# Performance work log

Hardware: AMD Instinct MI355X
Metric: run time of the kernel (lower is better)

The kernel has to match this reference:

```python
import jax, jax.numpy as jnp
import numpy as np

N = 100000   # nodes
E = 1250000  # edges per graph
D = 64       # in_feats
H = 64       # hidden_dim
C = 129      # num_classes
EPS = 1e-5


def setup_inputs() -> dict:
    key = jax.random.key(0)
    ks = jax.random.split(key, 32)
    nrm = lambda k, s: jax.random.normal(k, s, jnp.float32) * 0.05
    inp = {
        'node_features': jax.random.normal(ks[0], (N, D), jnp.float32),
        'm_src': jax.random.randint(ks[1], (E,), 0, N, jnp.int32),
        'm_dst': jax.random.randint(ks[2], (E,), 0, N, jnp.int32),
        'r_src': jax.random.randint(ks[3], (E,), 0, N, jnp.int32),
        'r_dst': jax.random.randint(ks[4], (E,), 0, N, jnp.int32),
    }
    i = 5
    for pre in ('soc', 'rt'):
        inp[pre + '_W1'] = nrm(ks[i], (D, H)); inp[pre + '_b1'] = jnp.zeros((H,), jnp.float32)
        inp[pre + '_g1'] = jnp.ones((H,), jnp.float32); inp[pre + '_bt1'] = jnp.zeros((H,), jnp.float32)
        inp[pre + '_W2'] = nrm(ks[i + 1], (H, H)); inp[pre + '_b2'] = jnp.zeros((H,), jnp.float32)
        inp[pre + '_g2'] = jnp.ones((H,), jnp.float32); inp[pre + '_bt2'] = jnp.zeros((H,), jnp.float32)
        i += 2
    inp['gW1'] = nrm(ks[i], (4 * H, H)); inp['gb1'] = jnp.zeros((H,), jnp.float32)
    inp['prelu_a'] = jnp.full((1,), 0.25, jnp.float32)
    inp['gW2'] = nrm(ks[i + 1], (H, H)); inp['gb2'] = jnp.zeros((H,), jnp.float32)
    inp['fcW'] = nrm(ks[i + 2], (H, C)); inp['fcb'] = jnp.zeros((C,), jnp.float32)
    return inp


def _gconv(h, src, dst, W, b):
    # DGL GraphConv, norm='both': D_out^{-1/2} (scatter-sum) D_in^{-1/2}, linear, ELU
    ones = jnp.ones(src.shape[0], jnp.float32)
    deg_o = jax.ops.segment_sum(ones, src, num_segments=N)
    deg_i = jax.ops.segment_sum(ones, dst, num_segments=N)
    ns = jax.lax.rsqrt(jnp.clip(deg_o, 1.0))
    nd = jax.lax.rsqrt(jnp.clip(deg_i, 1.0))
    agg = jax.ops.segment_sum((h * ns[:, None])[src], dst, num_segments=N)
    return jax.nn.elu((agg * nd[:, None]) @ W + b)


def _bn(x, g, b):
    mu = x.mean(0)
    v = x.var(0)
    return (x - mu) * jax.lax.rsqrt(v + EPS) * g + b


def _branch(x, src, dst, W1, b1, g1, bt1, W2, b2, g2, bt2):
    h = _bn(_gconv(x, src, dst, W1, b1), g1, bt1)
    return _bn(_gconv(h, src, dst, W2, b2), g2, bt2)


def reference(node_features, m_src, m_dst, r_src, r_dst,
              soc_W1, soc_b1, soc_g1, soc_bt1, soc_W2, soc_b2, soc_g2, soc_bt2,
              rt_W1, rt_b1, rt_g1, rt_bt1, rt_W2, rt_b2, rt_g2, rt_bt2,
              gW1, gb1, prelu_a, gW2, gb2, fcW, fcb):
    h1 = _branch(node_features, m_src, m_dst, soc_W1, soc_b1, soc_g1, soc_bt1, soc_W2, soc_b2, soc_g2, soc_bt2)
    h2 = _branch(node_features, r_src, r_dst, rt_W1, rt_b1, rt_g1, rt_bt1, rt_W2, rt_b2, rt_g2, rt_bt2)
    cat = jnp.concatenate([h1, h2, jnp.abs(h1 - h2), h1 * h2], axis=-1)
    z = cat @ gW1 + gb1
    z = jnp.where(z > 0, z, prelu_a * z)  # PReLU (single shared slope)
    gate = jax.nn.sigmoid(z @ gW2 + gb2)
    fused = gate * h1 + (1.0 - gate) * h2
    return fused @ fcW + fcb
```

## Files before the change

### kernel.cpp

```cpp
#include <hip/hip_runtime.h>
#include <math.h>

#define NN 100000
#define NE 1250000
#define HD 64
#define NCLS 129
#define NTILES 6250
#define GRID_T 782

#define NCHD 256
#define CHD ((NE + NCHD - 1) / NCHD)
#define NCHS 64
#define CHS ((NE + NCHS - 1) / NCHS)
#define SUBR 50000
#define NW2 12500
#define NHE2 ((NN + 1) * (size_t)HD)

typedef float f32x4 __attribute__((ext_vector_type(4)));
typedef short bf16x8 __attribute__((ext_vector_type(8)));

__device__ __forceinline__ short f2b(float f) {
    unsigned u = __builtin_bit_cast(unsigned, f);
    u += 0x7FFFu + ((u >> 16) & 1u);
    return (short)(u >> 16);
}
__device__ __forceinline__ float b2f(short s) {
    return __builtin_bit_cast(float, ((unsigned)(unsigned short)s) << 16);
}

__global__ __launch_bounds__(1024) void k_hist8(
    const int* __restrict__ idx0, const int* __restrict__ idx1,
    unsigned char* __restrict__ P8, int chunk, int nch) {
    __shared__ unsigned int hw[NW2];
    int b = blockIdx.x, s = blockIdx.y, g = blockIdx.z;
    const int* __restrict__ idx = g ? idx1 : idx0;
    for (int i = threadIdx.x; i < NW2; i += 1024) hw[i] = 0;
    __syncthreads();
    int lo = s * SUBR;
    int beg = b * chunk, end = beg + chunk;
    if (end > NE) end = NE;
    for (int i = beg + threadIdx.x; i < end; i += 1024) {
        int v = idx[i] - lo;
        if ((unsigned)v < (unsigned)SUBR)
            atomicAdd(&hw[v >> 2], 1u << ((v & 3) * 8));
    }
    __syncthreads();
    unsigned int* dst = (unsigned int*)(P8 + ((size_t)(g * nch + b)) * NN + lo);
    for (int i = threadIdx.x; i < NW2; i += 1024) dst[i] = hw[i];
}

__global__ void k_reduce8(unsigned int* __restrict__ Pd, const unsigned int* __restrict__ Ps,
                          float* __restrict__ ns, float* __restrict__ nd,
                          int* __restrict__ degi) {
    int w = blockIdx.x * 256 + threadIdx.x;
    if (w >= NN / 4) return;
    int g = blockIdx.y;
    Pd += (size_t)g * NCHD * (NN / 4);
    Ps += (size_t)g * NCHS * (NN / 4);
    ns += (size_t)g * NN; nd += (size_t)g * NN; degi += (size_t)g * NN;
    unsigned run = 0;
#pragma unroll 8
    for (int b = 0; b < NCHD; ++b) {
        size_t o = (size_t)b * (NN / 4) + w;
        unsigned v = Pd[o];
        Pd[o] = run;
        run += v;
    }
    unsigned so = 0;
#pragma unroll 8
    for (int b = 0; b < NCHS; ++b) so += Ps[(size_t)b * (NN / 4) + w];
#pragma unroll
    for (int j = 0; j < 4; ++j) {
        int din = (run >> (8 * j)) & 255;
        int dout = (so >> (8 * j)) & 255;
        int node = w * 4 + j;
        degi[node] = din;
        ns[node] = rsqrtf((float)(dout < 1 ? 1 : dout));
        nd[node] = rsqrtf((float)(din < 1 ? 1 : din));
    }
}

__global__ void k_scan_local(const int* __restrict__ deg, int* __restrict__ excl,
                             int* __restrict__ bsums) {
    __shared__ int sm[1024];
    int g = blockIdx.y;
    deg += (size_t)g * NN; excl += (size_t)g * (NN + 1); bsums += g * 1024;
    int t = threadIdx.x;
    int i = blockIdx.x * 1024 + t;
    int v = (i < NN) ? deg[i] : 0;
    sm[t] = v;
    __syncthreads();
    for (int ofs = 1; ofs < 1024; ofs <<= 1) {
        int x = (t >= ofs) ? sm[t - ofs] : 0;
        __syncthreads();
        sm[t] += x;
        __syncthreads();
    }
    if (i < NN) excl[i] = sm[t] - v;
    if (t == 1023) bsums[blockIdx.x] = sm[1023];
}

__global__ void k_scan_tops(int* __restrict__ bsums, int nb) {
    __shared__ int sm[1024];
    bsums += blockIdx.y * 1024;
    int t = threadIdx.x;
    int v = (t < nb) ? bsums[t] : 0;
    sm[t] = v;
    __syncthreads();
    for (int ofs = 1; ofs < 1024; ofs <<= 1) {
        int x = (t >= ofs) ? sm[t - ofs] : 0;
        __syncthreads();
        sm[t] += x;
        __syncthreads();
    }
    if (t < nb) bsums[t] = sm[t] - v;
}

__global__ void k_scan_add(int* __restrict__ excl, const int* __restrict__ bsums) {
    int g = blockIdx.y;
    excl += (size_t)g * (NN + 1); bsums += g * 1024;
    int i = blockIdx.x * blockDim.x + threadIdx.x;
    if (i < NN) excl[i] += bsums[i >> 10];
    if (i == 0) excl[NN] = NE;
}

__global__ __launch_bounds__(1024) void k_fill8(
    const int* __restrict__ d0, const int* __restrict__ d1,
    const int* __restrict__ s0, const int* __restrict__ s1,
    const int* __restrict__ rowptr, const unsigned char* __restrict__ Pofs,
    int* __restrict__ col) {
    __shared__ unsigned int cur[NW2];
    int b = blockIdx.x, s = blockIdx.y, g = blockIdx.z;
    const int* __restrict__ dst = g ? d1 : d0;
    const int* __restrict__ src = g ? s1 : s0;
    rowptr += (size_t)g * (NN + 1);
    col += (size_t)g * NE;
    const unsigned char* __restrict__ ofs = Pofs + ((size_t)(g * NCHD + b)) * NN;
    for (int i = threadIdx.x; i < NW2; i += 1024) cur[i] = 0;
    __syncthreads();
    int lo = s * SUBR;
    int beg = b * CHD, end = beg + CHD;
    if (end > NE) end = NE;
    for (int i = beg + threadIdx.x; i < end; i += 1024) {
        int d = dst[i] - lo;
        if ((unsigned)d < (unsigned)SUBR) {
            unsigned old = atomicAdd(&cur[d >> 2], 1u << ((d & 3) * 8));
            int r = (old >> ((d & 3) * 8)) & 255;
            int node = d + lo;
            col[rowptr[node] + (int)ofs[node] + r] = src[i];
        }
    }
}

__global__ void k_scale_nf(const float* __restrict__ nf, const float* __restrict__ ns,
                           short* __restrict__ T) {
    int i = blockIdx.x * blockDim.x + threadIdx.x;
    if (i >= (NN + 1) * 8) return;
    int g = blockIdx.y;
    ns += (size_t)g * NN; T += (size_t)g * NHE2;
    int node = i >> 3;
    short r[8];
    if (node == NN) {
#pragma unroll
        for (int j = 0; j < 8; ++j) r[j] = 0;
    } else {
        float s = ns[node];
        const float4* p = (const float4*)(nf + (size_t)i * 8);
        float4 a = p[0], b = p[1];
        r[0] = f2b(a.x * s); r[1] = f2b(a.y * s); r[2] = f2b(a.z * s); r[3] = f2b(a.w * s);
        r[4] = f2b(b.x * s); r[5] = f2b(b.y * s); r[6] = f2b(b.z * s); r[7] = f2b(b.w * s);
    }
    *(bf16x8*)(T + (size_t)i * 8) = *(bf16x8*)r;
}

__global__ __launch_bounds__(256) void k_gather(
    const short* __restrict__ tab, const float* __restrict__ nd,
    const int* __restrict__ rowptr, const int* __restrict__ col,
    short* __restrict__ out) {
    int w = (blockIdx.x * 256 + threadIdx.x) >> 6;
    int lane = threadIdx.x & 63;
    if (w >= NN) return;
    int g = blockIdx.y;
    tab += (size_t)g * NHE2; nd += (size_t)g * NN;
    rowptr += (size_t)g * (NN + 1); col += (size_t)g * NE; out += (size_t)g * NHE2;
    int grp = lane >> 4;
    int sub = lane & 15;
    int beg = rowptr[w], end = rowptr[w + 1];
    float a0 = 0.f, a1 = 0.f, a2 = 0.f, a3 = 0.f;
    for (int e0 = beg; e0 < end; e0 += 64) {
        int cnt = end - e0; if (cnt > 64) cnt = 64;
        int myc = (lane < cnt) ? col[e0 + lane] : NN;
        for (int j = 0; j < cnt; j += 16) {
#pragma unroll
            for (int u = 0; u < 4; ++u) {
                int c = __shfl(myc, j + u * 4 + grp, 64);
                uint2 v = *(const uint2*)(tab + (size_t)c * HD + sub * 4);
                a0 += __builtin_bit_cast(float, v.x << 16);
                a1 += __builtin_bit_cast(float, v.x & 0xffff0000u);
                a2 += __builtin_bit_cast(float, v.y << 16);
                a3 += __builtin_bit_cast(float, v.y & 0xffff0000u);
            }
        }
    }
    a0 += __shfl_xor(a0, 16, 64); a1 += __shfl_xor(a1, 16, 64);
    a2 += __shfl_xor(a2, 16, 64); a3 += __shfl_xor(a3, 16, 64);
    a0 += __shfl_xor(a0, 32, 64); a1 += __shfl_xor(a1, 32, 64);
    a2 += __shfl_xor(a2, 32, 64); a3 += __shfl_xor(a3, 32, 64);
    if (grp == 0) {
        float s = nd[w];
        unsigned r0 = ((unsigned)(unsigned short)f2b(a0 * s)) |
                      (((unsigned)(unsigned short)f2b(a1 * s)) << 16);
        unsigned r1 = ((unsigned)(unsigned short)f2b(a2 * s)) |
                      (((unsigned)(unsigned short)f2b(a3 * s)) << 16);
        uint2 r; r.x = r0; r.y = r1;
        *(uint2*)(out + (size_t)w * HD + sub * 4) = r;
    }
}

__global__ __launch_bounds__(256) void k_lin(
    const short* __restrict__ X, const float* __restrict__ Wa, const float* __restrict__ Wb,
    const float* __restrict__ ba, const float* __restrict__ bb,
    short* __restrict__ Y, float* __restrict__ stats) {
    __shared__ short sW[4096];
    __shared__ float sm2[128];
    int g = blockIdx.y;
    const float* W = g ? Wb : Wa;
    const float* bias = g ? bb : ba;
    X += (size_t)g * NHE2; Y += (size_t)g * NHE2; stats += (size_t)g * 128;
    int t = threadIdx.x;
    for (int i = t; i < 4096; i += 256) {
        int j = i & 7, l16i = (i >> 3) & 15, kgi = (i >> 7) & 3, kbi = (i >> 9) & 1, oti = (i >> 10) & 3;
        sW[i] = f2b(W[(kbi * 32 + kgi * 8 + j) * HD + oti * 16 + l16i]);
    }
    if (t < 128) sm2[t] = 0.f;
    __syncthreads();
    int lane = t & 63, wv = t >> 6, l16 = lane & 15, kg = lane >> 4;
    bf16x8 bfrag[2][4];
#pragma unroll
    for (int kb = 0; kb < 2; ++kb)
#pragma unroll
        for (int ot = 0; ot < 4; ++ot)
            bfrag[kb][ot] = *(const bf16x8*)&sW[((ot * 2 + kb) * 4 + kg) * 128 + l16 * 8];
    float bo[4];
#pragma unroll
    for (int ot = 0; ot < 4; ++ot) bo[ot] = bias[ot * 16 + l16];
    float ps[4] = {0.f, 0.f, 0.f, 0.f}, pq[4] = {0.f, 0.f, 0.f, 0.f};
    for (int tile = blockIdx.x * 4 + wv; tile < NTILES; tile += GRID_T * 4) {
        const short* xp = X + ((size_t)tile * 16 + l16) * HD + kg * 8;
        bf16x8 a0 = *(const bf16x8*)xp;
        bf16x8 a1 = *(const bf16x8*)(xp + 32);
        f32x4 acc[4];
#pragma unroll
        for (int ot = 0; ot < 4; ++ot) {
            acc[ot] = (f32x4){0.f, 0.f, 0.f, 0.f};
            acc[ot] = __builtin_amdgcn_mfma_f32_16x16x32_bf16(a0, bfrag[0][ot], acc[ot], 0, 0, 0);
            acc[ot] = __builtin_amdgcn_mfma_f32_16x16x32_bf16(a1, bfrag[1][ot], acc[ot], 0, 0, 0);
        }
#pragma unroll
        for (int ot = 0; ot < 4; ++ot) {
#pragma unroll
            for (int r = 0; r < 4; ++r) {
                float y = acc[ot][r] + bo[ot];
                y = y > 0.f ? y : expm1f(y);
                ps[ot] += y; pq[ot] += y * y;
                Y[((size_t)tile * 16 + kg * 4 + r) * HD + ot * 16 + l16] = f2b(y);
            }
        }
    }
#pragma unroll
    for (int ot = 0; ot < 4; ++ot) {
        atomicAdd(&sm2[ot * 16 + l16], ps[ot]);
        atomicAdd(&sm2[64 + ot * 16 + l16], pq[ot]);
    }
    __syncthreads();
    if (t < 128) atomicAdd(&stats[t], sm2[t]);
}

__global__ void k_bnb(const short* __restrict__ Y, short* __restrict__ O,
                      const float* __restrict__ stats,
                      const float* __restrict__ ga, const float* __restrict__ gb,
                      const float* __restrict__ bta, const float* __restrict__ btb,
                      const float* __restrict__ ns) {
    int i = blockIdx.x * blockDim.x + threadIdx.x;
    if (i >= (NN + 1) * 8) return;
    int gI = blockIdx.y;
    Y += (size_t)gI * NHE2; O += (size_t)gI * NHE2; stats += (size_t)gI * 128;
    const float* g = gI ? gb : ga;
    const float* bt = gI ? btb : bta;
    if (ns) ns += (size_t)gI * NN;
    int node = i >> 3;
    short r[8];
    if (node == NN) {
#pragma unroll
        for (int j = 0; j < 8; ++j) r[j] = 0;
    } else {
        int o0 = (i & 7) * 8;
        float extra = ns ? ns[node] : 1.f;
        bf16x8 v = *(const bf16x8*)(Y + (size_t)i * 8);
        const float invN = 1.f / (float)NN;
#pragma unroll
        for (int j = 0; j < 8; ++j) {
            int o = o0 + j;
            float mu = stats[o] * invN;
            float var = fmaxf(stats[64 + o] * invN - mu * mu, 0.f);
            float isd = rsqrtf(var + 1e-5f);
            float sc = g[o] * isd * extra;
            float sh = (bt[o] - mu * g[o] * isd) * extra;
            r[j] = f2b(b2f(v[j]) * sc + sh);
        }
    }
    *(bf16x8*)(O + (size_t)i * 8) = *(bf16x8*)r;
}

__global__ __launch_bounds__(256) void k_comb1(
    const short* __restrict__ H1, const short* __restrict__ H2,
    const float* __restrict__ W, const float* __restrict__ bias,
    const float* __restrict__ pa, short* __restrict__ Z) {
    __shared__ short sW[16384];
    int t = threadIdx.x;
    for (int i = t; i < 16384; i += 256) {
        int j = i & 7, l16i = (i >> 3) & 15, kgi = (i >> 7) & 3, kbi = (i >> 9) & 7, oti = (i >> 12) & 3;
        sW[i] = f2b(W[(kbi * 32 + kgi * 8 + j) * HD + oti * 16 + l16i]);
    }
    __syncthreads();
    int lane = t & 63, wv = t >> 6, l16 = lane & 15, kg = lane >> 4;
    float slope = pa[0];
    float bo[4];
#pragma unroll
    for (int ot = 0; ot < 4; ++ot) bo[ot] = bias[ot * 16 + l16];
    for (int tile = blockIdx.x * 4 + wv; tile < NTILES; tile += GRID_T * 4) {
        size_t rb = ((size_t)tile * 16 + l16) * HD + kg * 8;
        bf16x8 h1e = *(const bf16x8*)(H1 + rb);
        bf16x8 h1o = *(const bf16x8*)(H1 + rb + 32);
        bf16x8 h2e = *(const bf16x8*)(H2 + rb);
        bf16x8 h2o = *(const bf16x8*)(H2 + rb + 32);
        bf16x8 fe[8];
        fe[0] = h1e; fe[1] = h1o; fe[2] = h2e; fe[3] = h2o;
        short tabs[8], tprd[8];
#pragma unroll
        for (int j = 0; j < 8; ++j) {
            float a = b2f(h1e[j]), b = b2f(h2e[j]);
            tabs[j] = f2b(fabsf(a - b)); tprd[j] = f2b(a * b);
        }
        fe[4] = *(bf16x8*)tabs; fe[6] = *(bf16x8*)tprd;
#pragma unroll
        for (int j = 0; j < 8; ++j) {
            float a = b2f(h1o[j]), b = b2f(h2o[j]);
            tabs[j] = f2b(fabsf(a - b)); tprd[j] = f2b(a * b);
        }
        fe[5] = *(bf16x8*)tabs; fe[7] = *(bf16x8*)tprd;
        f32x4 acc[4];
#pragma unroll
        for (int ot = 0; ot < 4; ++ot) acc[ot] = (f32x4){0.f, 0.f, 0.f, 0.f};
#pragma unroll
        for (int kb = 0; kb < 8; ++kb)
#pragma unroll
            for (int ot = 0; ot < 4; ++ot) {
                bf16x8 bf = *(const bf16x8*)&sW[((ot * 8 + kb) * 4 + kg) * 128 + l16 * 8];
                acc[ot] = __builtin_amdgcn_mfma_f32_16x16x32_bf16(fe[kb], bf, acc[ot], 0, 0, 0);
            }
#pragma unroll
        for (int ot = 0; ot < 4; ++ot)
#pragma unroll
            for (int r = 0; r < 4; ++r) {
                float z = acc[ot][r] + bo[ot];
                z = z > 0.f ? z : slope * z;
                Z[((size_t)tile * 16 + kg * 4 + r) * HD + ot * 16 + l16] = f2b(z);
            }
    }
}

__global__ __launch_bounds__(256) void k_comb2(
    const short* __restrict__ Z, const float* __restrict__ W,
    const float* __restrict__ bias, short* __restrict__ G) {
    __shared__ short sW[4096];
    int t = threadIdx.x;
    for (int i = t; i < 4096; i += 256) {
        int j = i & 7, l16i = (i >> 3) & 15, kgi = (i >> 7) & 3, kbi = (i >> 9) & 1, oti = (i >> 10) & 3;
        sW[i] = f2b(W[(kbi * 32 + kgi * 8 + j) * HD + oti * 16 + l16i]);
    }
    __syncthreads();
    int lane = t & 63, wv = t >> 6, l16 = lane & 15, kg = lane >> 4;
    bf16x8 bfrag[2][4];
#pragma unroll
    for (int kb = 0; kb < 2; ++kb)
#pragma unroll
        for (int ot = 0; ot < 4; ++ot)
            bfrag[kb][ot] = *(const bf16x8*)&sW[((ot * 2 + kb) * 4 + kg) * 128 + l16 * 8];
    float bo[4];
#pragma unroll
    for (int ot = 0; ot < 4; ++ot) bo[ot] = bias[ot * 16 + l16];
    for (int tile = blockIdx.x * 4 + wv; tile < NTILES; tile += GRID_T * 4) {
        const short* xp = Z + ((size_t)tile * 16 + l16) * HD + kg * 8;
        bf16x8 a0 = *(const bf16x8*)xp;
        bf16x8 a1 = *(const bf16x8*)(xp + 32);
        f32x4 acc[4];
#pragma unroll
        for (int ot = 0; ot < 4; ++ot) {
            acc[ot] = (f32x4){0.f, 0.f, 0.f, 0.f};
            acc[ot] = __builtin_amdgcn_mfma_f32_16x16x32_bf16(a0, bfrag[0][ot], acc[ot], 0, 0, 0);
            acc[ot] = __builtin_amdgcn_mfma_f32_16x16x32_bf16(a1, bfrag[1][ot], acc[ot], 0, 0, 0);
        }
#pragma unroll
        for (int ot = 0; ot < 4; ++ot)
#pragma unroll
            for (int r = 0; r < 4; ++r) {
                float y = acc[ot][r] + bo[ot];
                float gate = 1.f / (1.f + expf(-y));
                G[((size_t)tile * 16 + kg * 4 + r) * HD + ot * 16 + l16] = f2b(gate);
            }
    }
}

__global__ __launch_bounds__(256) void k_fc(
    const short* __restrict__ G, const short* __restrict__ H1, const short* __restrict__ H2,
    const float* __restrict__ W, const float* __restrict__ bias,
    float* __restrict__ out) {
    __shared__ short sW[9216];
    int t = threadIdx.x;
    for (int i = t; i < 9216; i += 256) {
        int j = i & 7, l16i = (i >> 3) & 15, kgi = (i >> 7) & 3, kbi = (i >> 9) & 1, oti = i >> 10;
        int k = kbi * 32 + kgi * 8 + j, o = oti * 16 + l16i;
        sW[i] = (o < NCLS) ? f2b(W[k * NCLS + o]) : (short)0;
    }
    __syncthreads();
    int lane = t & 63, wv = t >> 6, l16 = lane & 15, kg = lane >> 4;
    float bo[9];
#pragma unroll
    for (int ot = 0; ot < 9; ++ot) {
        int o = ot * 16 + l16;
        bo[ot] = (o < NCLS) ? bias[o] : 0.f;
    }
    for (int tile = blockIdx.x * 4 + wv; tile < NTILES; tile += GRID_T * 4) {
        size_t rb = ((size_t)tile * 16 + l16) * HD;
        f32x4 acc[9];
#pragma unroll
        for (int ot = 0; ot < 9; ++ot) acc[ot] = (f32x4){0.f, 0.f, 0.f, 0.f};
#pragma unroll
        for (int kb = 0; kb < 2; ++kb) {
            int koff = kb * 32 + kg * 8;
            bf16x8 gv  = *(const bf16x8*)(G + rb + koff);
            bf16x8 h1v = *(const bf16x8*)(H1 + rb + koff);
            bf16x8 h2v = *(const bf16x8*)(H2 + rb + koff);
            short af[8];
#pragma unroll
            for (int j = 0; j < 8; ++j) {
                float gf = b2f(gv[j]);
                af[j] = f2b(gf * b2f(h1v[j]) + (1.f - gf) * b2f(h2v[j]));
            }
            bf16x8 a = *(bf16x8*)af;
#pragma unroll
            for (int ot = 0; ot < 9; ++ot) {
                bf16x8 bf = *(const bf16x8*)&sW[((ot * 2 + kb) * 4 + kg) * 128 + l16 * 8];
                acc[ot] = __builtin_amdgcn_mfma_f32_16x16x32_bf16(a, bf, acc[ot], 0, 0, 0);
            }
        }
#pragma unroll
        for (int ot = 0; ot < 9; ++ot) {
            int o = ot * 16 + l16;
            if (o < NCLS) {
#pragma unroll
                for (int r = 0; r < 4; ++r) {
                    int node = tile * 16 + kg * 4 + r;
                    out[(size_t)node * NCLS + o] = acc[ot][r] + bo[ot];
                }
            }
        }
    }
}

extern "C" void kernel_launch(void* const* d_in, const int* in_sizes, int n_in,
                              void* d_out, int out_size, void* d_ws, size_t ws_size,
                              hipStream_t stream) {
    (void)in_sizes; (void)n_in; (void)out_size; (void)ws_size;
    const int N = NN;

    const float* nf = (const float*)d_in[0];
    const int* m_src = (const int*)d_in[1];
    const int* m_dst = (const int*)d_in[2];
    const int* r_src = (const int*)d_in[3];
    const int* r_dst = (const int*)d_in[4];
    const float *W1[2], *b1[2], *g1[2], *bt1[2], *W2[2], *b2[2], *g2[2], *bt2[2];
    for (int br = 0; br < 2; ++br) {
        int base = 5 + br * 8;
        W1[br] = (const float*)d_in[base + 0];
        b1[br] = (const float*)d_in[base + 1];
        g1[br] = (const float*)d_in[base + 2];
        bt1[br] = (const float*)d_in[base + 3];
        W2[br] = (const float*)d_in[base + 4];
        b2[br] = (const float*)d_in[base + 5];
        g2[br] = (const float*)d_in[base + 6];
        bt2[br] = (const float*)d_in[base + 7];
    }
    const float* gW1 = (const float*)d_in[21];
    const float* gb1 = (const float*)d_in[22];
    const float* pa  = (const float*)d_in[23];
    const float* gW2 = (const float*)d_in[24];
    const float* gb2 = (const float*)d_in[25];
    const float* fcW = (const float*)d_in[26];
    const float* fcb = (const float*)d_in[27];
    float* out = (float*)d_out;

    char* p = (char*)d_ws;
    auto take = [&](size_t bytes) { char* r = p; p += (bytes + 255) & ~(size_t)255; return r; };
    size_t NHb2 = NHE2 * 2;
    unsigned char* P8d = (unsigned char*)take((size_t)2 * NCHD * NN);
    unsigned char* P8s = (unsigned char*)take((size_t)2 * NCHS * NN);
    short* T   = (short*)take(2 * NHb2);
    short* X   = (short*)take(2 * NHb2);
    short* Y   = (short*)take(2 * NHb2);
    short* Hs  = (short*)take(2 * NHb2);
    short* H   = (short*)take(2 * NHb2);
    float* ns = (float*)take((size_t)2 * N * 4);
    float* nd = (float*)take((size_t)2 * N * 4);
    float* stats = (float*)take(2 * 2 * 128 * 4);
    int* degi = (int*)take((size_t)2 * N * 4);
    int* rowptr = (int*)take((size_t)2 * (N + 1) * 4);
    int* bsums = (int*)take(2 * 4096);
    short* Z = (short*)d_out;
    int* col = (int*)((char*)d_out + (size_t)N * HD * 2);

    int gN = (N + 255) / 256;
    int nScanBlk = (N + 1023) / 1024;
    int gEW = ((N + 1) * 8 + 255) / 256;
    int gW4 = (N / 4 + 255) / 256;
    int gGat = (N * 64) / 256;

    k_hist8<<<dim3(NCHD, 2, 2), 1024, 0, stream>>>(m_dst, r_dst, P8d, CHD, NCHD);
    k_hist8<<<dim3(NCHS, 2, 2), 1024, 0, stream>>>(m_src, r_src, P8s, CHS, NCHS);
    k_reduce8<<<dim3(gW4, 2), 256, 0, stream>>>((unsigned int*)P8d, (const unsigned int*)P8s,
                                                ns, nd, degi);
    k_scan_local<<<dim3(nScanBlk, 2), 1024, 0, stream>>>(degi, rowptr, bsums);
    k_scan_tops<<<dim3(1, 2), 1024, 0, stream>>>(bsums, nScanBlk);
    k_scan_add<<<dim3(gN, 2), 256, 0, stream>>>(rowptr, bsums);
    k_fill8<<<dim3(NCHD, 2, 2), 1024, 0, stream>>>(m_dst, r_dst, m_src, r_src, rowptr, P8d, col);
    hipMemsetAsync(stats, 0, 2 * 2 * 128 * 4, stream);

    k_scale_nf<<<dim3(gEW, 2), 256, 0, stream>>>(nf, ns, T);
    k_gather<<<dim3(gGat, 2), 256, 0, stream>>>(T, nd, rowptr, col, X);
    k_lin<<<dim3(GRID_T, 2), 256, 0, stream>>>(X, W1[0], W1[1], b1[0], b1[1], Y, stats);
    k_bnb<<<dim3(gEW, 2), 256, 0, stream>>>(Y, Hs, stats, g1[0], g1[1], bt1[0], bt1[1], ns);

    k_gather<<<dim3(gGat, 2), 256, 0, stream>>>(Hs, nd, rowptr, col, X);
    k_lin<<<dim3(GRID_T, 2), 256, 0, stream>>>(X, W2[0], W2[1], b2[0], b2[1], Y, stats + 256);
    k_bnb<<<dim3(gEW, 2), 256, 0, stream>>>(Y, H, stats + 256, g2[0], g2[1], bt2[0], bt2[1],
                                            (const float*)nullptr);

    k_comb1<<<GRID_T, 256, 0, stream>>>(H, H + NHE2, gW1, gb1, pa, Z);
    k_comb2<<<GRID_T, 256, 0, stream>>>(Z, gW2, gb2, X);
    k_fc<<<GRID_T, 256, 0, stream>>>(X, H, H + NHE2, fcW, fcb, out);
}
```

Before: 446.0 us.

## Fuse gate/fc tail kernels, share node-feature table, merge histograms, reduce chunk count

```diff
diff --git a/kernel.cpp b/kernel.cpp
--- a/kernel.cpp
+++ b/kernel.cpp
@@ -8,10 +8,8 @@
 #define NTILES 6250
 #define GRID_T 782
 
-#define NCHD 256
-#define CHD ((NE + NCHD - 1) / NCHD)
-#define NCHS 64
-#define CHS ((NE + NCHS - 1) / NCHS)
+#define NCH 64
+#define CHU ((NE + NCH - 1) / NCH)
 #define SUBR 50000
 #define NW2 12500
 #define NHE2 ((NN + 1) * (size_t)HD)
@@ -29,15 +27,17 @@
 }
 
 __global__ __launch_bounds__(1024) void k_hist8(
-    const int* __restrict__ idx0, const int* __restrict__ idx1,
-    unsigned char* __restrict__ P8, int chunk, int nch) {
+    const int* __restrict__ d0, const int* __restrict__ s0,
+    const int* __restrict__ d1, const int* __restrict__ s1,
+    unsigned char* __restrict__ P8d, unsigned char* __restrict__ P8s) {
     __shared__ unsigned int hw[NW2];
-    int b = blockIdx.x, s = blockIdx.y, g = blockIdx.z;
-    const int* __restrict__ idx = g ? idx1 : idx0;
+    int b = blockIdx.x, s = blockIdx.y, z = blockIdx.z;
+    int g = z >> 1, arr = z & 1;
+    const int* __restrict__ idx = arr ? (g ? s1 : s0) : (g ? d1 : d0);
     for (int i = threadIdx.x; i < NW2; i += 1024) hw[i] = 0;
     __syncthreads();
     int lo = s * SUBR;
-    int beg = b * chunk, end = beg + chunk;
+    int beg = b * CHU, end = beg + CHU;
     if (end > NE) end = NE;
     for (int i = beg + threadIdx.x; i < end; i += 1024) {
         int v = idx[i] - lo;
@@ -45,7 +45,8 @@
             atomicAdd(&hw[v >> 2], 1u << ((v & 3) * 8));
     }
     __syncthreads();
-    unsigned int* dst = (unsigned int*)(P8 + ((size_t)(g * nch + b)) * NN + lo);
+    unsigned char* base = arr ? P8s : P8d;
+    unsigned int* dst = (unsigned int*)(base + ((size_t)(g * NCH + b)) * NN + lo);
     for (int i = threadIdx.x; i < NW2; i += 1024) dst[i] = hw[i];
 }
 
@@ -55,12 +56,13 @@
     int w = blockIdx.x * 256 + threadIdx.x;
     if (w >= NN / 4) return;
     int g = blockIdx.y;
-    Pd += (size_t)g * NCHD * (NN / 4);
-    Ps += (size_t)g * NCHS * (NN / 4);
-    ns += (size_t)g * NN; nd += (size_t)g * NN; degi += (size_t)g * NN;
+    Pd += (size_t)g * NCH * (NN / 4);
+    Ps += (size_t)g * NCH * (NN / 4);
+    ns += (size_t)g * (NN + 1); nd += (size_t)g * NN; degi += (size_t)g * NN;
+    if (w == 0) ns[NN] = 0.f;
     unsigned run = 0;
 #pragma unroll 8
-    for (int b = 0; b < NCHD; ++b) {
+    for (int b = 0; b < NCH; ++b) {
         size_t o = (size_t)b * (NN / 4) + w;
         unsigned v = Pd[o];
         Pd[o] = run;
@@ -68,7 +70,7 @@
     }
     unsigned so = 0;
 #pragma unroll 8
-    for (int b = 0; b < NCHS; ++b) so += Ps[(size_t)b * (NN / 4) + w];
+    for (int b = 0; b < NCH; ++b) so += Ps[(size_t)b * (NN / 4) + w];
 #pragma unroll
     for (int j = 0; j < 4; ++j) {
         int din = (run >> (8 * j)) & 255;
@@ -135,11 +137,11 @@
     const int* __restrict__ src = g ? s1 : s0;
     rowptr += (size_t)g * (NN + 1);
     col += (size_t)g * NE;
-    const unsigned char* __restrict__ ofs = Pofs + ((size_t)(g * NCHD + b)) * NN;
+    const unsigned char* __restrict__ ofs = Pofs + ((size_t)(g * NCH + b)) * NN;
     for (int i = threadIdx.x; i < NW2; i += 1024) cur[i] = 0;
     __syncthreads();
     int lo = s * SUBR;
-    int beg = b * CHD, end = beg + CHD;
+    int beg = b * CHU, end = beg + CHU;
     if (end > NE) end = NE;
     for (int i = beg + threadIdx.x; i < end; i += 1024) {
         int d = dst[i] - lo;
@@ -152,37 +154,35 @@
     }
 }
 
-__global__ void k_scale_nf(const float* __restrict__ nf, const float* __restrict__ ns,
-                           short* __restrict__ T) {
+__global__ void k_scale_nf(const float* __restrict__ nf, short* __restrict__ T) {
     int i = blockIdx.x * blockDim.x + threadIdx.x;
     if (i >= (NN + 1) * 8) return;
-    int g = blockIdx.y;
-    ns += (size_t)g * NN; T += (size_t)g * NHE2;
     int node = i >> 3;
     short r[8];
     if (node == NN) {
 #pragma unroll
         for (int j = 0; j < 8; ++j) r[j] = 0;
     } else {
-        float s = ns[node];
         const float4* p = (const float4*)(nf + (size_t)i * 8);
         float4 a = p[0], b = p[1];
-        r[0] = f2b(a.x * s); r[1] = f2b(a.y * s); r[2] = f2b(a.z * s); r[3] = f2b(a.w * s);
-        r[4] = f2b(b.x * s); r[5] = f2b(b.y * s); r[6] = f2b(b.z * s); r[7] = f2b(b.w * s);
+        r[0] = f2b(a.x); r[1] = f2b(a.y); r[2] = f2b(a.z); r[3] = f2b(a.w);
+        r[4] = f2b(b.x); r[5] = f2b(b.y); r[6] = f2b(b.z); r[7] = f2b(b.w);
     }
     *(bf16x8*)(T + (size_t)i * 8) = *(bf16x8*)r;
 }
 
+template <int NS>
 __global__ __launch_bounds__(256) void k_gather(
-    const short* __restrict__ tab, const float* __restrict__ nd,
-    const int* __restrict__ rowptr, const int* __restrict__ col,
-    short* __restrict__ out) {
+    const short* __restrict__ tab, size_t tabStride, const float* __restrict__ ns,
+    const float* __restrict__ nd, const int* __restrict__ rowptr,
+    const int* __restrict__ col, short* __restrict__ out) {
     int w = (blockIdx.x * 256 + threadIdx.x) >> 6;
     int lane = threadIdx.x & 63;
     if (w >= NN) return;
     int g = blockIdx.y;
-    tab += (size_t)g * NHE2; nd += (size_t)g * NN;
+    tab += (size_t)g * tabStride; nd += (size_t)g * NN;
     rowptr += (size_t)g * (NN + 1); col += (size_t)g * NE; out += (size_t)g * NHE2;
+    const float* nsA = ns + (size_t)g * (NN + 1);
     int grp = lane >> 4;
     int sub = lane & 15;
     int beg = rowptr[w], end = rowptr[w + 1];
@@ -190,15 +190,25 @@
     for (int e0 = beg; e0 < end; e0 += 64) {
         int cnt = end - e0; if (cnt > 64) cnt = 64;
         int myc = (lane < cnt) ? col[e0 + lane] : NN;
+        float myns = 0.f;
+        if (NS) myns = nsA[myc];
         for (int j = 0; j < cnt; j += 16) {
 #pragma unroll
             for (int u = 0; u < 4; ++u) {
-                int c = __shfl(myc, j + u * 4 + grp, 64);
+                int idx = j + u * 4 + grp;
+                int c = __shfl(myc, idx, 64);
                 uint2 v = *(const uint2*)(tab + (size_t)c * HD + sub * 4);
-                a0 += __builtin_bit_cast(float, v.x << 16);
-                a1 += __builtin_bit_cast(float, v.x & 0xffff0000u);
-                a2 += __builtin_bit_cast(float, v.y << 16);
-                a3 += __builtin_bit_cast(float, v.y & 0xffff0000u);
+                float v0 = __builtin_bit_cast(float, v.x << 16);
+                float v1 = __builtin_bit_cast(float, v.x & 0xffff0000u);
+                float v2 = __builtin_bit_cast(float, v.y << 16);
+                float v3 = __builtin_bit_cast(float, v.y & 0xffff0000u);
+                if (NS) {
+                    float nsc = __shfl(myns, idx, 64);
+                    a0 = fmaf(nsc, v0, a0); a1 = fmaf(nsc, v1, a1);
+                    a2 = fmaf(nsc, v2, a2); a3 = fmaf(nsc, v3, a3);
+                } else {
+                    a0 += v0; a1 += v1; a2 += v2; a3 += v3;
+                }
             }
         }
     }
@@ -287,7 +297,7 @@
     Y += (size_t)gI * NHE2; O += (size_t)gI * NHE2; stats += (size_t)gI * 128;
     const float* g = gI ? gb : ga;
     const float* bt = gI ? btb : bta;
-    if (ns) ns += (size_t)gI * NN;
+    if (ns) ns += (size_t)gI * (NN + 1);
     int node = i >> 3;
     short r[8];
     if (node == NN) {
@@ -312,22 +322,52 @@
     *(bf16x8*)(O + (size_t)i * 8) = *(bf16x8*)r;
 }
 
-__global__ __launch_bounds__(256) void k_comb1(
+#define TRS 72
+__global__ __launch_bounds__(256) void k_tail(
     const short* __restrict__ H1, const short* __restrict__ H2,
-    const float* __restrict__ W, const float* __restrict__ bias,
-    const float* __restrict__ pa, short* __restrict__ Z) {
-    __shared__ short sW[16384];
+    const float* __restrict__ W1, const float* __restrict__ bias1,
+    const float* __restrict__ pa,
+    const float* __restrict__ W2, const float* __restrict__ bias2,
+    const float* __restrict__ Wf, const float* __restrict__ biasf,
+    float* __restrict__ out) {
+    __shared__ short sW1[16384];
+    __shared__ short sW2[4096];
+    __shared__ short sWf[9216];
+    __shared__ short tr[4][2][16 * TRS];
     int t = threadIdx.x;
     for (int i = t; i < 16384; i += 256) {
         int j = i & 7, l16i = (i >> 3) & 15, kgi = (i >> 7) & 3, kbi = (i >> 9) & 7, oti = (i >> 12) & 3;
-        sW[i] = f2b(W[(kbi * 32 + kgi * 8 + j) * HD + oti * 16 + l16i]);
+        sW1[i] = f2b(W1[(kbi * 32 + kgi * 8 + j) * HD + oti * 16 + l16i]);
+    }
+    for (int i = t; i < 4096; i += 256) {
+        int j = i & 7, l16i = (i >> 3) & 15, kgi = (i >> 7) & 3, kbi = (i >> 9) & 1, oti = (i >> 10) & 3;
+        sW2[i] = f2b(W2[(kbi * 32 + kgi * 8 + j) * HD + oti * 16 + l16i]);
+    }
+    for (int i = t; i < 9216; i += 256) {
+        int j = i & 7, l16i = (i >> 3) & 15, kgi = (i >> 7) & 3, kbi = (i >> 9) & 1, oti = i >> 10;
+        int k = kbi * 32 + kgi * 8 + j, o = oti * 16 + l16i;
+        sWf[i] = (o < NCLS) ? f2b(Wf[k * NCLS + o]) : (short)0;
     }
     __syncthreads();
     int lane = t & 63, wv = t >> 6, l16 = lane & 15, kg = lane >> 4;
     float slope = pa[0];
-    float bo[4];
-#pragma unroll
-    for (int ot = 0; ot < 4; ++ot) bo[ot] = bias[ot * 16 + l16];
+    float bo1[4], bo2[4], bof[9];
+#pragma unroll
+    for (int ot = 0; ot < 4; ++ot) { bo1[ot] = bias1[ot * 16 + l16]; bo2[ot] = bias2[ot * 16 + l16]; }
+#pragma unroll
+    for (int ot = 0; ot < 9; ++ot) {
+        int o = ot * 16 + l16;
+        bof[ot] = (o < NCLS) ? biasf[o] : 0.f;
+    }
+    bf16x8 b2frag[2][4];
+#pragma unroll
+    for (int kb = 0; kb < 2; ++kb)
+#pragma unroll
+        for (int ot = 0; ot < 4; ++ot)
+            b2frag[kb][ot] = *(const bf16x8*)&sW2[((ot * 2 + kb) * 4 + kg) * 128 + l16 * 8];
+    short* trZ = &tr[wv][0][0];
+    short* trG = &tr[wv][1][0];
+
     for (int tile = blockIdx.x * 4 + wv; tile < NTILES; tile += GRID_T * 4) {
         size_t rb = ((size_t)tile * 16 + l16) * HD + kg * 8;
         bf16x8 h1e = *(const bf16x8*)(H1 + rb);
@@ -356,103 +396,59 @@
         for (int kb = 0; kb < 8; ++kb)
 #pragma unroll
             for (int ot = 0; ot < 4; ++ot) {
-                bf16x8 bf = *(const bf16x8*)&sW[((ot * 8 + kb) * 4 + kg) * 128 + l16 * 8];
+                bf16x8 bf = *(const bf16x8*)&sW1[((ot * 8 + kb) * 4 + kg) * 128 + l16 * 8];
                 acc[ot] = __builtin_amdgcn_mfma_f32_16x16x32_bf16(fe[kb], bf, acc[ot], 0, 0, 0);
             }
 #pragma unroll
         for (int ot = 0; ot < 4; ++ot)
 #pragma unroll
             for (int r = 0; r < 4; ++r) {
-                float z = acc[ot][r] + bo[ot];
+                float z = acc[ot][r] + bo1[ot];
                 z = z > 0.f ? z : slope * z;
-                Z[((size_t)tile * 16 + kg * 4 + r) * HD + ot * 16 + l16] = f2b(z);
-            }
-    }
-}
-
-__global__ __launch_bounds__(256) void k_comb2(
-    const short* __restrict__ Z, const float* __restrict__ W,
-    const float* __restrict__ bias, short* __restrict__ G) {
-    __shared__ short sW[4096];
-    int t = threadIdx.x;
-    for (int i = t; i < 4096; i += 256) {
-        int j = i & 7, l16i = (i >> 3) & 15, kgi = (i >> 7) & 3, kbi = (i >> 9) & 1, oti = (i >> 10) & 3;
-        sW[i] = f2b(W[(kbi * 32 + kgi * 8 + j) * HD + oti * 16 + l16i]);
-    }
-    __syncthreads();
-    int lane = t & 63, wv = t >> 6, l16 = lane & 15, kg = lane >> 4;
-    bf16x8 bfrag[2][4];
-#pragma unroll
-    for (int kb = 0; kb < 2; ++kb)
+                trZ[(kg * 4 + r) * TRS + ot * 16 + l16] = f2b(z);
+            }
+        asm volatile("s_waitcnt lgkmcnt(0)" ::: "memory");
+        __builtin_amdgcn_sched_barrier(0);
+        bf16x8 za0 = *(const bf16x8*)&trZ[l16 * TRS + kg * 8];
+        bf16x8 za1 = *(const bf16x8*)&trZ[l16 * TRS + 32 + kg * 8];
+        f32x4 acc2[4];
+#pragma unroll
+        for (int ot = 0; ot < 4; ++ot) {
+            acc2[ot] = (f32x4){0.f, 0.f, 0.f, 0.f};
+            acc2[ot] = __builtin_amdgcn_mfma_f32_16x16x32_bf16(za0, b2frag[0][ot], acc2[ot], 0, 0, 0);
+            acc2[ot] = __builtin_amdgcn_mfma_f32_16x16x32_bf16(za1, b2frag[1][ot], acc2[ot], 0, 0, 0);
+        }
 #pragma unroll
         for (int ot = 0; ot < 4; ++ot)
-            bfrag[kb][ot] = *(const bf16x8*)&sW[((ot * 2 + kb) * 4 + kg) * 128 + l16 * 8];
-    float bo[4];
-#pragma unroll
-    for (int ot = 0; ot < 4; ++ot) bo[ot] = bias[ot * 16 + l16];
-    for (int tile = blockIdx.x * 4 + wv; tile < NTILES; tile += GRID_T * 4) {
-        const short* xp = Z + ((size_t)tile * 16 + l16) * HD + kg * 8;
-        bf16x8 a0 = *(const bf16x8*)xp;
-        bf16x8 a1 = *(const bf16x8*)(xp + 32);
-        f32x4 acc[4];
-#pragma unroll
-        for (int ot = 0; ot < 4; ++ot) {
-            acc[ot] = (f32x4){0.f, 0.f, 0.f, 0.f};
-            acc[ot] = __builtin_amdgcn_mfma_f32_16x16x32_bf16(a0, bfrag[0][ot], acc[ot], 0, 0, 0);
-            acc[ot] = __builtin_amdgcn_mfma_f32_16x16x32_bf16(a1, bfrag[1][ot], acc[ot], 0, 0, 0);
-        }
-#pragma unroll
-        for (int ot = 0; ot < 4; ++ot)
 #pragma unroll
             for (int r = 0; r < 4; ++r) {
-                float y = acc[ot][r] + bo[ot];
+                float y = acc2[ot][r] + bo2[ot];
                 float gate = 1.f / (1.f + expf(-y));
-                G[((size_t)tile * 16 + kg * 4 + r) * HD + ot * 16 + l16] = f2b(gate);
-            }
-    }
-}
-
-__global__ __launch_bounds__(256) void k_fc(
-    const short* __restrict__ G, const short* __restrict__ H1, const short* __restrict__ H2,
-    const float* __restrict__ W, const float* __restrict__ bias,
-    float* __restrict__ out) {
-    __shared__ short sW[9216];
-    int t = threadIdx.x;
-    for (int i = t; i < 9216; i += 256) {
-        int j = i & 7, l16i = (i >> 3) & 15, kgi = (i >> 7) & 3, kbi = (i >> 9) & 1, oti = i >> 10;
-        int k = kbi * 32 + kgi * 8 + j, o = oti * 16 + l16i;
-        sW[i] = (o < NCLS) ? f2b(W[k * NCLS + o]) : (short)0;
-    }
-    __syncthreads();
-    int lane = t & 63, wv = t >> 6, l16 = lane & 15, kg = lane >> 4;
-    float bo[9];
-#pragma unroll
-    for (int ot = 0; ot < 9; ++ot) {
-        int o = ot * 16 + l16;
-        bo[ot] = (o < NCLS) ? bias[o] : 0.f;
-    }
-    for (int tile = blockIdx.x * 4 + wv; tile < NTILES; tile += GRID_T * 4) {
-        size_t rb = ((size_t)tile * 16 + l16) * HD;
-        f32x4 acc[9];
-#pragma unroll
-        for (int ot = 0; ot < 9; ++ot) acc[ot] = (f32x4){0.f, 0.f, 0.f, 0.f};
+                trG[(kg * 4 + r) * TRS + ot * 16 + l16] = f2b(gate);
+            }
+        asm volatile("s_waitcnt lgkmcnt(0)" ::: "memory");
+        __builtin_amdgcn_sched_barrier(0);
+        bf16x8 ga0 = *(const bf16x8*)&trG[l16 * TRS + kg * 8];
+        bf16x8 ga1 = *(const bf16x8*)&trG[l16 * TRS + 32 + kg * 8];
+        short f0[8], f1[8];
+#pragma unroll
+        for (int j = 0; j < 8; ++j) {
+            float gf = b2f(ga0[j]);
+            f0[j] = f2b(gf * b2f(h1e[j]) + (1.f - gf) * b2f(h2e[j]));
+            float gf2 = b2f(ga1[j]);
+            f1[j] = f2b(gf2 * b2f(h1o[j]) + (1.f - gf2) * b2f(h2o[j]));
+        }
+        bf16x8 fa0 = *(bf16x8*)f0, fa1 = *(bf16x8*)f1;
+        f32x4 acc3[9];
+#pragma unroll
+        for (int ot = 0; ot < 9; ++ot) acc3[ot] = (f32x4){0.f, 0.f, 0.f, 0.f};
 #pragma unroll
         for (int kb = 0; kb < 2; ++kb) {
-            int koff = kb * 32 + kg * 8;
-            bf16x8 gv  = *(const bf16x8*)(G + rb + koff);
-            bf16x8 h1v = *(const bf16x8*)(H1 + rb + koff);
-            bf16x8 h2v = *(const bf16x8*)(H2 + rb + koff);
-            short af[8];
-#pragma unroll
-            for (int j = 0; j < 8; ++j) {
-                float gf = b2f(gv[j]);
-                af[j] = f2b(gf * b2f(h1v[j]) + (1.f - gf) * b2f(h2v[j]));
-            }
-            bf16x8 a = *(bf16x8*)af;
+            bf16x8 a = kb ? fa1 : fa0;
 #pragma unroll
             for (int ot = 0; ot < 9; ++ot) {
-                bf16x8 bf = *(const bf16x8*)&sW[((ot * 2 + kb) * 4 + kg) * 128 + l16 * 8];
-                acc[ot] = __builtin_amdgcn_mfma_f32_16x16x32_bf16(a, bf, acc[ot], 0, 0, 0);
+                bf16x8 bf = *(const bf16x8*)&sWf[((ot * 2 + kb) * 4 + kg) * 128 + l16 * 8];
+                acc3[ot] = __builtin_amdgcn_mfma_f32_16x16x32_bf16(a, bf, acc3[ot], 0, 0, 0);
             }
         }
 #pragma unroll
@@ -462,7 +458,7 @@
 #pragma unroll
                 for (int r = 0; r < 4; ++r) {
                     int node = tile * 16 + kg * 4 + r;
-                    out[(size_t)node * NCLS + o] = acc[ot][r] + bo[ot];
+                    out[(size_t)node * NCLS + o] = acc3[ot][r] + bof[ot];
                 }
             }
         }
@@ -504,20 +500,19 @@
     char* p = (char*)d_ws;
     auto take = [&](size_t bytes) { char* r = p; p += (bytes + 255) & ~(size_t)255; return r; };
     size_t NHb2 = NHE2 * 2;
-    unsigned char* P8d = (unsigned char*)take((size_t)2 * NCHD * NN);
-    unsigned char* P8s = (unsigned char*)take((size_t)2 * NCHS * NN);
-    short* T   = (short*)take(2 * NHb2);
+    unsigned char* P8d = (unsigned char*)take((size_t)2 * NCH * NN);
+    unsigned char* P8s = (unsigned char*)take((size_t)2 * NCH * NN);
+    short* T   = (short*)take(NHb2);
     short* X   = (short*)take(2 * NHb2);
     short* Y   = (short*)take(2 * NHb2);
     short* Hs  = (short*)take(2 * NHb2);
     short* H   = (short*)take(2 * NHb2);
-    float* ns = (float*)take((size_t)2 * N * 4);
+    float* ns = (float*)take((size_t)2 * (N + 1) * 4);
     float* nd = (float*)take((size_t)2 * N * 4);
     float* stats = (float*)take(2 * 2 * 128 * 4);
     int* degi = (int*)take((size_t)2 * N * 4);
     int* rowptr = (int*)take((size_t)2 * (N + 1) * 4);
     int* bsums = (int*)take(2 * 4096);
-    short* Z = (short*)d_out;
     int* col = (int*)((char*)d_out + (size_t)N * HD * 2);
 
     int gN = (N + 255) / 256;
@@ -526,27 +521,24 @@
     int gW4 = (N / 4 + 255) / 256;
     int gGat = (N * 64) / 256;
 
-    k_hist8<<<dim3(NCHD, 2, 2), 1024, 0, stream>>>(m_dst, r_dst, P8d, CHD, NCHD);
-    k_hist8<<<dim3(NCHS, 2, 2), 1024, 0, stream>>>(m_src, r_src, P8s, CHS, NCHS);
+    k_hist8<<<dim3(NCH, 2, 4), 1024, 0, stream>>>(m_dst, m_src, r_dst, r_src, P8d, P8s);
     k_reduce8<<<dim3(gW4, 2), 256, 0, stream>>>((unsigned int*)P8d, (const unsigned int*)P8s,
                                                 ns, nd, degi);
     k_scan_local<<<dim3(nScanBlk, 2), 1024, 0, stream>>>(degi, rowptr, bsums);
     k_scan_tops<<<dim3(1, 2), 1024, 0, stream>>>(bsums, nScanBlk);
     k_scan_add<<<dim3(gN, 2), 256, 0, stream>>>(rowptr, bsums);
-    k_fill8<<<dim3(NCHD, 2, 2), 1024, 0, stream>>>(m_dst, r_dst, m_src, r_src, rowptr, P8d, col);
+    k_fill8<<<dim3(NCH, 2, 2), 1024, 0, stream>>>(m_dst, r_dst, m_src, r_src, rowptr, P8d, col);
     hipMemsetAsync(stats, 0, 2 * 2 * 128 * 4, stream);
 
-    k_scale_nf<<<dim3(gEW, 2), 256, 0, stream>>>(nf, ns, T);
-    k_gather<<<dim3(gGat, 2), 256, 0, stream>>>(T, nd, rowptr, col, X);
+    k_scale_nf<<<gEW, 256, 0, stream>>>(nf, T);
+    k_gather<1><<<dim3(gGat, 2), 256, 0, stream>>>(T, 0, ns, nd, rowptr, col, X);
     k_lin<<<dim3(GRID_T, 2), 256, 0, stream>>>(X, W1[0], W1[1], b1[0], b1[1], Y, stats);
     k_bnb<<<dim3(gEW, 2), 256, 0, stream>>>(Y, Hs, stats, g1[0], g1[1], bt1[0], bt1[1], ns);
 
-    k_gather<<<dim3(gGat, 2), 256, 0, stream>>>(Hs, nd, rowptr, col, X);
+    k_gather<0><<<dim3(gGat, 2), 256, 0, stream>>>(Hs, NHE2, ns, nd, rowptr, col, X);
     k_lin<<<dim3(GRID_T, 2), 256, 0, stream>>>(X, W2[0], W2[1], b2[0], b2[1], Y, stats + 256);
     k_bnb<<<dim3(gEW, 2), 256, 0, stream>>>(Y, H, stats + 256, g2[0], g2[1], bt2[0], bt2[1],
                                             (const float*)nullptr);
 
-    k_comb1<<<GRID_T, 256, 0, stream>>>(H, H + NHE2, gW1, gb1, pa, Z);
-    k_comb2<<<GRID_T, 256, 0, stream>>>(Z, gW2, gb2, X);
-    k_fc<<<GRID_T, 256, 0, stream>>>(X, H, H + NHE2, fcW, fcb, out);
-}
+    k_tail<<<GRID_T, 256, 0, stream>>>(H, H + NHE2, gW1, gb1, pa, gW2, gb2, fcW, fcb, out);
+}
```

Result: faster. 391.3 us (-12.3%).
